# Performance work log

Hardware: AMD Instinct MI355X
Metric: run time of the kernel (lower is better)

## Reference

```python
import jax, jax.numpy as jnp
import numpy as np

N, IN, OUT = 262144, 256, 256
EPS_MIN = 1e-10


def setup_inputs() -> dict:
    key = jax.random.key(0)
    k1, k2, k3 = jax.random.split(key, 3)
    x = jax.random.normal(k1, (N, IN), dtype=jnp.float32)
    weight = jax.random.normal(k2, (OUT, IN), dtype=jnp.float32) * 0.05
    bias = jax.random.normal(k3, (OUT,), dtype=jnp.float32) * 0.02
    return {"x": x, "weight": weight, "bias": bias}


def reference(x, weight, bias):
    # Mean-center weight rows and input rows (dim=1 in torch)
    wc = weight - jnp.mean(weight, axis=1, keepdims=True)          # [out, in]
    xc = x - jnp.mean(x, axis=1, keepdims=True)                    # [N, in]
    # temp_linear with all-ones weight == row-sum of xc^2, broadcast over out
    x_len = jax.lax.stop_gradient(
        jnp.sqrt(jnp.sum(xc * xc, axis=1, keepdims=True)))          # [N, 1]
    # temp_linear(ones_like(x)) with weight wc^2 == row-sum of wc^2 per out
    w_len = jax.lax.stop_gradient(
        jnp.sqrt(jnp.sum(wc * wc, axis=1)))                          # [out]
    # Correlation: centered GEMM, normalized, clamped; bias added after clamp
    corr = jnp.einsum('ni,oi->no', xc, wc) / (x_len * w_len[None, :])
    out = jnp.clip(corr, EPS_MIN, None) + bias[None, :]
    return out
```

## Files before the change

kernel.cpp:

```cpp
#include <hip/hip_runtime.h>
#include <hip/hip_bf16.h>


#define K_DIM 256
#define N_OUT 256
#define BM 64
#define LDS_STRIDE 264

typedef __attribute__((ext_vector_type(8))) __bf16 bf16x8;
typedef __attribute__((ext_vector_type(4))) float f32x4;

__device__ __forceinline__ unsigned short f2bf(float f) {
    union { float f; unsigned u; } v; v.f = f;
    unsigned r = v.u + 0x7FFFu + ((v.u >> 16) & 1u);
    return (unsigned short)(r >> 16);
}

__global__ __launch_bounds__(64) void prep_w(const float* __restrict__ w,
                                             unsigned short* __restrict__ wcb) {
    int o = blockIdx.x;
    int lane = threadIdx.x;
    f32x4 v = *((const f32x4*)(w + (size_t)o * K_DIM) + lane);
    float s  = v.x + v.y + v.z + v.w;
    float s2 = v.x*v.x + v.y*v.y + v.z*v.z + v.w*v.w;
#pragma unroll
    for (int off = 32; off >= 1; off >>= 1) {
        s  += __shfl_xor(s,  off);
        s2 += __shfl_xor(s2, off);
    }
    float mean  = s * (1.0f / 256.0f);
    float var   = s2 - s * mean;
    float scale = rsqrtf(fmaxf(var, 1e-30f));
    ushort4 b;
    b.x = f2bf((v.x - mean) * scale);
    b.y = f2bf((v.y - mean) * scale);
    b.z = f2bf((v.z - mean) * scale);
    b.w = f2bf((v.w - mean) * scale);
    *(ushort4*)(wcb + (size_t)o * K_DIM + lane * 4) = b;
}

__global__ __launch_bounds__(256, 2) void pcc_gemm(const float* __restrict__ x,
                                                   const unsigned short* __restrict__ wcb,
                                                   const float* __restrict__ bias,
                                                   float* __restrict__ out) {
    __shared__ unsigned short xs[BM * LDS_STRIDE];

    const int t    = threadIdx.x;
    const int wave = t >> 6;
    const int lane = t & 63;
    const size_t row0 = (size_t)blockIdx.x * BM;

    const float* xbase = x + row0 * K_DIM;

#pragma unroll 2
    for (int it = 0; it < 16; ++it) {
        const int row = it * 4 + wave;
        f32x4 v = *((const f32x4*)(xbase + (size_t)row * K_DIM) + lane);
        float s  = v.x + v.y + v.z + v.w;
        float s2 = v.x*v.x + v.y*v.y + v.z*v.z + v.w*v.w;
#pragma unroll
        for (int off = 32; off >= 1; off >>= 1) {
            s  += __shfl_xor(s,  off);
            s2 += __shfl_xor(s2, off);
        }
        float var = s2 - s * s * (1.0f / 256.0f);
        float inv = rsqrtf(fmaxf(var, 1e-30f));
        ushort4 b;
        b.x = f2bf(v.x * inv);
        b.y = f2bf(v.y * inv);
        b.z = f2bf(v.z * inv);
        b.w = f2bf(v.w * inv);
        *(ushort4*)(xs + row * LDS_STRIDE + lane * 4) = b;
    }
    __syncthreads();

    const int l15  = lane & 15;
    const int quad = lane >> 4;
    const int n0   = wave * 64;

    f32x4 acc[4][4];
#pragma unroll
    for (int mi = 0; mi < 4; ++mi)
#pragma unroll
        for (int ni = 0; ni < 4; ++ni)
            acc[mi][ni] = (f32x4){0.f, 0.f, 0.f, 0.f};

    const unsigned short* wbase = wcb + (size_t)n0 * K_DIM + quad * 8;

#pragma unroll
    for (int ks = 0; ks < 8; ++ks) {
        bf16x8 a[4], b[4];
#pragma unroll
        for (int mi = 0; mi < 4; ++mi)
            a[mi] = *(const bf16x8*)(xs + (mi * 16 + l15) * LDS_STRIDE + ks * 32 + quad * 8);
#pragma unroll
        for (int ni = 0; ni < 4; ++ni)
            b[ni] = *(const bf16x8*)(wbase + (size_t)(ni * 16 + l15) * K_DIM + ks * 32);
#pragma unroll
        for (int mi = 0; mi < 4; ++mi)
#pragma unroll
            for (int ni = 0; ni < 4; ++ni)
                acc[mi][ni] = __builtin_amdgcn_mfma_f32_16x16x32_bf16(a[mi], b[ni], acc[mi][ni], 0, 0, 0);
    }

    float bv[4];
#pragma unroll
    for (int ni = 0; ni < 4; ++ni) bv[ni] = bias[n0 + ni * 16 + l15];

    float* obase = out + row0 * N_OUT;
#pragma unroll
    for (int mi = 0; mi < 4; ++mi) {
#pragma unroll
        for (int r = 0; r < 4; ++r) {
            const int orow = mi * 16 + quad * 4 + r;
            float* op = obase + (size_t)orow * N_OUT + n0 + l15;
#pragma unroll
            for (int ni = 0; ni < 4; ++ni)
                op[ni * 16] = fmaxf(acc[mi][ni][r], 1e-10f) + bv[ni];
        }
    }
}

extern "C" void kernel_launch(void* const* d_in, const int* in_sizes, int n_in,
                              void* d_out, int out_size, void* d_ws, size_t ws_size,
                              hipStream_t stream) {
    const float* x    = (const float*)d_in[0];
    const float* w    = (const float*)d_in[1];
    const float* bias = (const float*)d_in[2];
    float* out = (float*)d_out;
    unsigned short* wcb = (unsigned short*)d_ws;

    prep_w<<<256, 64, 0, stream>>>(w, wcb);
    pcc_gemm<<<262144 / BM, 256, 0, stream>>>(x, wcb, bias, out);
}
```

Measured before the change: 486.1 us.

## Load x rows fully up front and defer row normalization to GEMM epilogue

Each lane now loads a quarter row (16 float4 loads in flight) instead of one float4 per loop iteration, and converts the raw x values to bf16 without scaling. The per-row inverse norm goes to shared memory and is applied to the accumulator in the epilogue, which cuts the shuffle reduction from six steps to two. Launch bounds are raised to 4 blocks per CU to add occupancy. The 16 live float4 registers may strain the register budget under the tighter bound, and quantizing unscaled x to bf16 changes rounding slightly.

```diff
diff --git a/kernel.cpp b/kernel.cpp
--- a/kernel.cpp
+++ b/kernel.cpp
@@ -8,6 +8,7 @@
 #define LDS_STRIDE 264
 
 typedef __attribute__((ext_vector_type(8))) __bf16 bf16x8;
+typedef __attribute__((ext_vector_type(8))) unsigned short u16x8;
 typedef __attribute__((ext_vector_type(4))) float f32x4;
 
 __device__ __forceinline__ unsigned short f2bf(float f) {
@@ -39,44 +40,58 @@
     *(ushort4*)(wcb + (size_t)o * K_DIM + lane * 4) = b;
 }
 
-__global__ __launch_bounds__(256, 2) void pcc_gemm(const float* __restrict__ x,
+__global__ __launch_bounds__(256, 4) void pcc_gemm(const float* __restrict__ x,
                                                    const unsigned short* __restrict__ wcb,
                                                    const float* __restrict__ bias,
                                                    float* __restrict__ out) {
     __shared__ unsigned short xs[BM * LDS_STRIDE];
+    __shared__ float nrm[BM];
 
     const int t    = threadIdx.x;
     const int wave = t >> 6;
     const int lane = t & 63;
+    const int l15  = lane & 15;
+    const int q    = lane >> 4;
     const size_t row0 = (size_t)blockIdx.x * BM;
 
-    const float* xbase = x + row0 * K_DIM;
+    const int srow = wave * 16 + l15;
+    const float* rp = x + (row0 + srow) * K_DIM + q * 64;
 
-#pragma unroll 2
-    for (int it = 0; it < 16; ++it) {
-        const int row = it * 4 + wave;
-        f32x4 v = *((const f32x4*)(xbase + (size_t)row * K_DIM) + lane);
-        float s  = v.x + v.y + v.z + v.w;
-        float s2 = v.x*v.x + v.y*v.y + v.z*v.z + v.w*v.w;
+    f32x4 v[16];
 #pragma unroll
-        for (int off = 32; off >= 1; off >>= 1) {
-            s  += __shfl_xor(s,  off);
-            s2 += __shfl_xor(s2, off);
-        }
-        float var = s2 - s * s * (1.0f / 256.0f);
-        float inv = rsqrtf(fmaxf(var, 1e-30f));
-        ushort4 b;
-        b.x = f2bf(v.x * inv);
-        b.y = f2bf(v.y * inv);
-        b.z = f2bf(v.z * inv);
-        b.w = f2bf(v.w * inv);
-        *(ushort4*)(xs + row * LDS_STRIDE + lane * 4) = b;
+    for (int j = 0; j < 16; ++j) v[j] = ((const f32x4*)rp)[j];
+
+    const int n0 = wave * 64;
+    float bv[4];
+#pragma unroll
+    for (int ni = 0; ni < 4; ++ni) bv[ni] = bias[n0 + ni * 16 + l15];
+
+    unsigned short* wp = xs + srow * LDS_STRIDE + q * 64;
+#pragma unroll
+    for (int j = 0; j < 8; ++j) {
+        u16x8 p;
+        p[0] = f2bf(v[2*j].x);   p[1] = f2bf(v[2*j].y);
+        p[2] = f2bf(v[2*j].z);   p[3] = f2bf(v[2*j].w);
+        p[4] = f2bf(v[2*j+1].x); p[5] = f2bf(v[2*j+1].y);
+        p[6] = f2bf(v[2*j+1].z); p[7] = f2bf(v[2*j+1].w);
+        *(u16x8*)(wp + j * 8) = p;
     }
+
+    float s = 0.f, s2 = 0.f;
+#pragma unroll
+    for (int j = 0; j < 16; ++j) {
+        s += v[j].x + v[j].y + v[j].z + v[j].w;
+        s2 = fmaf(v[j].x, v[j].x, s2);
+        s2 = fmaf(v[j].y, v[j].y, s2);
+        s2 = fmaf(v[j].z, v[j].z, s2);
+        s2 = fmaf(v[j].w, v[j].w, s2);
+    }
+    s  += __shfl_xor(s, 16);  s  += __shfl_xor(s, 32);
+    s2 += __shfl_xor(s2, 16); s2 += __shfl_xor(s2, 32);
+    float var = s2 - s * s * (1.0f / 256.0f);
+    float inv = rsqrtf(fmaxf(var, 1e-30f));
+    if (q == 0) nrm[srow] = inv;
     __syncthreads();
-
-    const int l15  = lane & 15;
-    const int quad = lane >> 4;
-    const int n0   = wave * 64;
 
     f32x4 acc[4][4];
 #pragma unroll
@@ -85,14 +100,14 @@
         for (int ni = 0; ni < 4; ++ni)
             acc[mi][ni] = (f32x4){0.f, 0.f, 0.f, 0.f};
 
-    const unsigned short* wbase = wcb + (size_t)n0 * K_DIM + quad * 8;
+    const unsigned short* wbase = wcb + (size_t)n0 * K_DIM + q * 8;
 
 #pragma unroll
     for (int ks = 0; ks < 8; ++ks) {
         bf16x8 a[4], b[4];
 #pragma unroll
         for (int mi = 0; mi < 4; ++mi)
-            a[mi] = *(const bf16x8*)(xs + (mi * 16 + l15) * LDS_STRIDE + ks * 32 + quad * 8);
+            a[mi] = *(const bf16x8*)(xs + (mi * 16 + l15) * LDS_STRIDE + ks * 32 + q * 8);
 #pragma unroll
         for (int ni = 0; ni < 4; ++ni)
             b[ni] = *(const bf16x8*)(wbase + (size_t)(ni * 16 + l15) * K_DIM + ks * 32);
@@ -103,20 +118,23 @@
                 acc[mi][ni] = __builtin_amdgcn_mfma_f32_16x16x32_bf16(a[mi], b[ni], acc[mi][ni], 0, 0, 0);
     }
 
-    float bv[4];
+    float invv[4][4];
 #pragma unroll
-    for (int ni = 0; ni < 4; ++ni) bv[ni] = bias[n0 + ni * 16 + l15];
+    for (int mi = 0; mi < 4; ++mi)
+#pragma unroll
+        for (int r = 0; r < 4; ++r)
+            invv[mi][r] = nrm[mi * 16 + q * 4 + r];
 
     float* obase = out + row0 * N_OUT;
 #pragma unroll
     for (int mi = 0; mi < 4; ++mi) {
 #pragma unroll
         for (int r = 0; r < 4; ++r) {
-            const int orow = mi * 16 + quad * 4 + r;
+            const int orow = mi * 16 + q * 4 + r;
             float* op = obase + (size_t)orow * N_OUT + n0 + l15;
 #pragma unroll
             for (int ni = 0; ni < 4; ++ni)
-                op[ni * 16] = fmaxf(acc[mi][ni][r], 1e-10f) + bv[ni];
+                op[ni * 16] = fmaxf(acc[mi][ni][r] * invv[mi][r], 1e-10f) + bv[ni];
         }
     }
 }
```

Result: faster. 474.8 us (-2.3%).
